# Kernel optimization log

Measured on AMD Instinct MI355X. Metric: run time of the kernel, lower is better.

The kernel has to match this reference:

```python
import jax, jax.numpy as jnp
import numpy as np
from jax import lax

COST_CLASS, COST_BBOX, COST_GIOU = 1.0, 5.0, 2.0


def box_cxcywh_to_xyxy(b):
    cx, cy, w, h = b[..., 0], b[..., 1], b[..., 2], b[..., 3]
    return jnp.stack([cx - 0.5 * w, cy - 0.5 * h, cx + 0.5 * w, cy + 0.5 * h], axis=-1)


def generalized_box_iou(boxes1, boxes2):
    # boxes1: [Q,4] xyxy, boxes2: [T,4] xyxy -> [Q,T]
    area1 = (boxes1[:, 2] - boxes1[:, 0]) * (boxes1[:, 3] - boxes1[:, 1])
    area2 = (boxes2[:, 2] - boxes2[:, 0]) * (boxes2[:, 3] - boxes2[:, 1])
    lt = jnp.maximum(boxes1[:, None, :2], boxes2[None, :, :2])  # [Q,T,2]
    rb = jnp.minimum(boxes1[:, None, 2:], boxes2[None, :, 2:])
    wh = jnp.clip(rb - lt, 0.0)
    inter = wh[..., 0] * wh[..., 1]
    union = area1[:, None] + area2[None, :] - inter
    iou = inter / union
    # smallest enclosing box
    lt_c = jnp.minimum(boxes1[:, None, :2], boxes2[None, :, :2])
    rb_c = jnp.maximum(boxes1[:, None, 2:], boxes2[None, :, 2:])
    wh_c = jnp.clip(rb_c - lt_c, 0.0)
    area_c = wh_c[..., 0] * wh_c[..., 1]
    return iou - (area_c - union) / area_c


def cost_matrix(logits, pboxes, labels, tboxes):
    # logits [Q,C], pboxes [Q,4], labels [T], tboxes [T,4] -> C [Q,T]
    prob = jax.nn.softmax(logits, axis=-1)
    cost_class = -prob[:, labels]                                  # [Q,T]
    cost_bbox = jnp.sum(jnp.abs(pboxes[:, None] - tboxes[None]), axis=-1)  # L1 cdist
    giou = generalized_box_iou(box_cxcywh_to_xyxy(pboxes), box_cxcywh_to_xyxy(tboxes))
    return COST_CLASS * cost_class + COST_BBOX * cost_bbox - COST_GIOU * giou


def greedy_match(C):
    # sequential greedy global-argmin matching, T steps (T <= Q)
    Q, T = C.shape

    def step(Cc, _):
        flat = jnp.argmin(Cc)
        i, j = flat // T, flat % T
        Cc = Cc.at[i, :].set(jnp.inf).at[:, j].set(jnp.inf)
        return Cc, (i.astype(jnp.int32), j.astype(jnp.int32))

    _, (src, tgt) = lax.scan(step, C, None, length=T)
    return src, tgt


def setup_inputs() -> dict:
    key = jax.random.key(0)
    k1, k2, k3, k4 = jax.random.split(key, 4)
    B, Q, C, T = 64, 900, 91, 128
    return {
        "pred_logits": jax.random.normal(k1, (B, Q, C), dtype=jnp.float32),
        "pred_boxes": jax.random.uniform(k2, (B, Q, 4), dtype=jnp.float32),
        "tgt_labels": jax.random.randint(k3, (B, T), 0, C, dtype=jnp.int32),
        "tgt_boxes": jax.random.uniform(k4, (B, T, 4), dtype=jnp.float32),
    }


def reference(pred_logits, pred_boxes, tgt_labels, tgt_boxes):
    C = jax.vmap(cost_matrix)(pred_logits, pred_boxes, tgt_labels, tgt_boxes)  # [B,Q,T]
    src_idx, tgt_idx = jax.vmap(greedy_match)(C)  # [B,T] each
    return src_idx, tgt_idx, C
```

## Files before the change

### kernel.cpp

```cpp
#include <hip/hip_runtime.h>
#include <cstdint>
#include <math.h>

#define NQ 900
#define NT 128
#define NC 91
#define KROWS 15
#define NCH 10

typedef unsigned long long u64;
typedef unsigned int u32;

__device__ __forceinline__ u32 fmono(float f){
  u32 u = __float_as_uint(f);
  return (u & 0x80000000u) ? ~u : (u | 0x80000000u);
}
__device__ __forceinline__ float fmono_inv(u32 m){
  u32 u = (m & 0x80000000u) ? (m & 0x7FFFFFFFu) : ~m;
  return __uint_as_float(u);
}

__device__ __forceinline__ u32 wave_argmin(float lv, u32 lm, float* gout){
  float x = lv;
  #define FSTG(C,RM) { int t_ = __builtin_amdgcn_update_dpp(__float_as_int(x), __float_as_int(x), C, RM, 0xf, false); x = fminf(x, __int_as_float(t_)); }
  FSTG(0x111,0xf) FSTG(0x112,0xf) FSTG(0x114,0xf) FSTG(0x118,0xf)
  FSTG(0x142,0xa) FSTG(0x143,0xc)
  #undef FSTG
  float gv = __int_as_float(__builtin_amdgcn_readlane(__float_as_int(x), 63));
  *gout = gv;
  u64 tie = __ballot(lv == gv);
  if (__popcll(tie) == 1){
    int w = (int)__ffsll((long long)tie) - 1;
    return (u32)__builtin_amdgcn_readlane((int)lm, w);
  }
  u32 m = (lv == gv) ? lm : 0xFFFFFFFFu;
  #define USTG(C,RM) { u32 t_ = (u32)__builtin_amdgcn_update_dpp((int)m, (int)m, C, RM, 0xf, false); m = t_ < m ? t_ : m; }
  USTG(0x111,0xf) USTG(0x112,0xf) USTG(0x114,0xf) USTG(0x118,0xf)
  USTG(0x142,0xa) USTG(0x143,0xc)
  #undef USTG
  return (u32)__builtin_amdgcn_readlane((int)m, 63);
}

__global__ __launch_bounds__(256) void cost_kernel(const float* __restrict__ logits,
                                                   const float* __restrict__ pboxes,
                                                   const int*   __restrict__ labels,
                                                   const float* __restrict__ tboxes,
                                                   float* __restrict__ Cout){
#pragma clang fp contract(off)
  int blk = blockIdx.x, tid = threadIdx.x;
  int idx = blk * 256 + tid;
  int t   = idx & (NT - 1);
  int bq  = idx >> 7;
  int b   = bq / NQ;
  int wid = tid >> 6, lane = tid & 63;

  __shared__ float sm_m[2], sm_s[2];
  if ((wid & 1) == 0){
    int r = blk * 2 + (wid >> 1);
    const float* row = logits + (size_t)r * NC;
    float v0 = (lane      < NC) ? row[lane]      : -INFINITY;
    float v1 = (lane + 64 < NC) ? row[lane + 64] : -INFINITY;
    float m = fmaxf(v0, v1);
    #pragma unroll
    for (int off = 32; off; off >>= 1) m = fmaxf(m, __shfl_xor(m, off));
    float s = ((lane < NC) ? expf(v0 - m) : 0.0f)
            + ((lane + 64 < NC) ? expf(v1 - m) : 0.0f);
    #pragma unroll
    for (int off = 32; off; off >>= 1) s += __shfl_xor(s, off);
    if (lane == 0){ sm_m[wid >> 1] = m; sm_s[wid >> 1] = s; }
  }
  __syncthreads();
  float m = sm_m[tid >> 7], s = sm_s[tid >> 7];

  int   lab = labels[b*NT + t];
  float l   = logits[(size_t)bq*NC + lab];
  float cclass = -(expf(l - m) / s);

  const float* pb = pboxes + (size_t)bq*4;
  const float* tb = tboxes + ((size_t)b*NT + t)*4;
  float pcx = pb[0], pcy = pb[1], pw = pb[2], ph = pb[3];
  float tcx = tb[0], tcy = tb[1], tw = tb[2], th = tb[3];

  float cbbox = ((fabsf(pcx-tcx) + fabsf(pcy-tcy)) + fabsf(pw-tw)) + fabsf(ph-th);

  float px0 = pcx - 0.5f*pw, py0 = pcy - 0.5f*ph;
  float px1 = pcx + 0.5f*pw, py1 = pcy + 0.5f*ph;
  float tx0 = tcx - 0.5f*tw, ty0 = tcy - 0.5f*th;
  float tx1 = tcx + 0.5f*tw, ty1 = tcy + 0.5f*th;

  float area1 = (px1 - px0) * (py1 - py0);
  float area2 = (tx1 - tx0) * (ty1 - ty0);
  float ltx = fmaxf(px0, tx0), lty = fmaxf(py0, ty0);
  float rbx = fminf(px1, tx1), rby = fminf(py1, ty1);
  float wx = fmaxf(rbx - ltx, 0.0f), wy = fmaxf(rby - lty, 0.0f);
  float inter = wx * wy;
  float uni   = (area1 + area2) - inter;
  float iou   = inter / uni;
  float cx0 = fminf(px0, tx0), cy0 = fminf(py0, ty0);
  float cx1 = fmaxf(px1, tx1), cy1 = fmaxf(py1, ty1);
  float cwx = fmaxf(cx1 - cx0, 0.0f), cwy = fmaxf(cy1 - cy0, 0.0f);
  float areac = cwx * cwy;
  float giou  = iou - (areac - uni) / areac;

  float cost = (cclass + 5.0f*cbbox) - 2.0f*giou;
  Cout[idx] = cost;
}

__global__ __launch_bounds__(128) void colmin_kernel(const float* __restrict__ Cmat,
                                                     u64* __restrict__ part){
  int b  = blockIdx.x / NCH;
  int ch = blockIdx.x - b * NCH;
  int t  = threadIdx.x;
  const float* Cb = Cmat + (size_t)b * NQ * NT + t;
  int r0 = ch * (NQ / NCH);
  u64 best = ~0ull;
  #pragma unroll 6
  for (int r = r0; r < r0 + NQ/NCH; ++r){
    float v = Cb[(size_t)r * NT];
    u64 k = ((u64)fmono(v) << 32) | (u32)r;
    best = k < best ? k : best;
  }
  part[((size_t)b * NCH + ch) * NT + t] = best;
}

__global__ __launch_bounds__(64) void greedy_kernel(const float* __restrict__ Cmat,
                                                    const u64* __restrict__ part,
                                                    float* __restrict__ outsrc,
                                                    float* __restrict__ outtgt){
  const int b    = blockIdx.x;
  const int lane = threadIdx.x;
  const float* Cb = Cmat + (size_t)b * NQ * NT;
  const u32 colA = 2*lane, colB = 2*lane + 1;

  u64 kA = ~0ull, kB = ~0ull;
  #pragma unroll
  for (int ch = 0; ch < NCH; ++ch){
    ulonglong2 p = ((const ulonglong2*)(part + ((size_t)b * NCH + ch) * NT))[lane];
    kA = p.x < kA ? p.x : kA;
    kB = p.y < kB ? p.y : kB;
  }
  float vA = fmono_inv((u32)(kA >> 32));
  float vB = fmono_inv((u32)(kB >> 32));
  u32 mA = ((((u32)kA) & 0x3FFu) << 7) | colA;
  u32 mB = ((((u32)kB) & 0x3FFu) << 7) | colB;

  u64 rd[KROWS];
  #pragma unroll
  for (int k = 0; k < KROWS; ++k) rd[k] = 0;

  for (int step = 0; step < NT; ++step){
    u32 gm;
    while (true){
      bool bsel = (vB < vA) || ((vB == vA) && (mB < mA));
      float lv = bsel ? vB : vA;
      u32   lm = bsel ? mB : mA;
      float gv;
      u32 g = wave_argmin(lv, lm, &gv);
      if (!(g >> 24)){ gm = g; break; }

      int jj = (int)(g & 0x7Fu);
      float w1 = INFINITY; u32 s1 = 0;
      #pragma unroll
      for (int k = 0; k < KROWS; ++k){
        int r = lane + 64*k;
        if (r < NQ){
          float v = Cb[(size_t)r * NT + jj];
          bool dead = ((rd[k] >> lane) & 1ull) != 0ull;
          v = dead ? INFINITY : v;
          if (v < w1){ w1 = v; s1 = (u32)r; }
        }
      }
      float rgv;
      u32 rrow = wave_argmin(w1, s1, &rgv);
      if (lane == (jj >> 1)){
        if (jj & 1){ vB = rgv; mB = (rrow << 7) | (u32)jj; }
        else       { vA = rgv; mA = (rrow << 7) | (u32)jj; }
      }
    }

    int i = (int)((gm >> 7) & 0x3FFu);
    int j = (int)(gm & 0x7Fu);
    if (lane == 0){
      outsrc[b*NT + step] = (float)i;
      outtgt[b*NT + step] = (float)j;
    }

    #pragma unroll
    for (int k = 0; k < KROWS; ++k)
      if ((i >> 6) == k) rd[k] |= (1ull << (i & 63));

    if (lane == (j >> 1)){
      if (j & 1){ vB = INFINITY; mB = 0x00FFFFFFu & ~(1u<<24); mB = 0x00FFFFFFu; }
      else      { vA = INFINITY; mA = 0x00FFFFFFu; }
    }
    if (((mA >> 7) & 0x3FFu) == (u32)i) mA |= (1u << 24);
    if (((mB >> 7) & 0x3FFu) == (u32)i) mB |= (1u << 24);
  }
}

extern "C" void kernel_launch(void* const* d_in, const int* in_sizes, int n_in,
                              void* d_out, int out_size, void* d_ws, size_t ws_size,
                              hipStream_t stream){
  const float* logits = (const float*)d_in[0];
  const float* pboxes = (const float*)d_in[1];
  const int*   labels = (const int*)  d_in[2];
  const float* tboxes = (const float*)d_in[3];
  int B = in_sizes[0] / (NQ * NC);

  float* out    = (float*)d_out;
  float* outsrc = out;
  float* outtgt = out + (size_t)B * NT;
  float* Cmat   = out + (size_t)2 * B * NT;

  u64* part = (u64*)d_ws;

  int nblk = (B * NQ) / 2;
  cost_kernel<<<nblk, 256, 0, stream>>>(logits, pboxes, labels, tboxes, Cmat);

  colmin_kernel<<<B * NCH, 128, 0, stream>>>(Cmat, part);

  greedy_kernel<<<B, 64, 0, stream>>>(Cmat, part, outsrc, outtgt);
}
```

Baseline: 246.0 us.

## Fuse cost and column-min kernels, split softmax stats, dual-pop greedy steps

Softmax row statistics move into their own kernel, and the cost computation is fused with the per-chunk column-min reduction, so the cost matrix is no longer re-read by a separate colmin pass. The greedy kernel now tries to commit two matches per iteration when the second argmin cannot conflict with the first. Outputs are buffered in registers and written once at the end. In exchange, the fused kernel launches only B*NCH blocks of 128 threads, far fewer than the old cost kernel, so the GPU may be underfilled. The dual-pop hazard logic also adds correctness risk.

Result: slower. 281.2 us (+14.3%).

```diff
diff --git a/kernel.cpp b/kernel.cpp
--- a/kernel.cpp
+++ b/kernel.cpp
@@ -7,6 +7,7 @@
 #define NC 91
 #define KROWS 15
 #define NCH 10
+#define RPC 90
 
 typedef unsigned long long u64;
 typedef unsigned int u32;
@@ -41,86 +42,75 @@
   return (u32)__builtin_amdgcn_readlane((int)m, 63);
 }
 
-__global__ __launch_bounds__(256) void cost_kernel(const float* __restrict__ logits,
-                                                   const float* __restrict__ pboxes,
-                                                   const int*   __restrict__ labels,
-                                                   const float* __restrict__ tboxes,
-                                                   float* __restrict__ Cout){
+__global__ void softmax_stats_kernel(const float* __restrict__ logits,
+                                     float* __restrict__ stats, int nrows){
+  int gw   = (int)((blockIdx.x * blockDim.x + threadIdx.x) >> 6);
+  int lane = threadIdx.x & 63;
+  if (gw >= nrows) return;
+  const float* row = logits + (size_t)gw * NC;
+  float v0 = (lane      < NC) ? row[lane]      : -INFINITY;
+  float v1 = (lane + 64 < NC) ? row[lane + 64] : -INFINITY;
+  float m = fmaxf(v0, v1);
+  #pragma unroll
+  for (int off = 32; off; off >>= 1) m = fmaxf(m, __shfl_xor(m, off));
+  float s = ((lane < NC) ? expf(v0 - m) : 0.0f)
+          + ((lane + 64 < NC) ? expf(v1 - m) : 0.0f);
+  #pragma unroll
+  for (int off = 32; off; off >>= 1) s += __shfl_xor(s, off);
+  if (lane == 0){ stats[2*gw] = m; stats[2*gw+1] = s; }
+}
+
+__global__ __launch_bounds__(128) void cost_colmin_kernel(
+    const float* __restrict__ logits, const float* __restrict__ pboxes,
+    const int*   __restrict__ labels, const float* __restrict__ tboxes,
+    const float* __restrict__ stats,  float* __restrict__ Cout,
+    u64* __restrict__ part){
 #pragma clang fp contract(off)
-  int blk = blockIdx.x, tid = threadIdx.x;
-  int idx = blk * 256 + tid;
-  int t   = idx & (NT - 1);
-  int bq  = idx >> 7;
-  int b   = bq / NQ;
-  int wid = tid >> 6, lane = tid & 63;
-
-  __shared__ float sm_m[2], sm_s[2];
-  if ((wid & 1) == 0){
-    int r = blk * 2 + (wid >> 1);
-    const float* row = logits + (size_t)r * NC;
-    float v0 = (lane      < NC) ? row[lane]      : -INFINITY;
-    float v1 = (lane + 64 < NC) ? row[lane + 64] : -INFINITY;
-    float m = fmaxf(v0, v1);
-    #pragma unroll
-    for (int off = 32; off; off >>= 1) m = fmaxf(m, __shfl_xor(m, off));
-    float s = ((lane < NC) ? expf(v0 - m) : 0.0f)
-            + ((lane + 64 < NC) ? expf(v1 - m) : 0.0f);
-    #pragma unroll
-    for (int off = 32; off; off >>= 1) s += __shfl_xor(s, off);
-    if (lane == 0){ sm_m[wid >> 1] = m; sm_s[wid >> 1] = s; }
-  }
-  __syncthreads();
-  float m = sm_m[tid >> 7], s = sm_s[tid >> 7];
+  int blk = blockIdx.x;
+  int b = blk / NCH, ch = blk - b * NCH;
+  int t = threadIdx.x;
 
   int   lab = labels[b*NT + t];
-  float l   = logits[(size_t)bq*NC + lab];
-  float cclass = -(expf(l - m) / s);
-
-  const float* pb = pboxes + (size_t)bq*4;
-  const float* tb = tboxes + ((size_t)b*NT + t)*4;
-  float pcx = pb[0], pcy = pb[1], pw = pb[2], ph = pb[3];
-  float tcx = tb[0], tcy = tb[1], tw = tb[2], th = tb[3];
-
-  float cbbox = ((fabsf(pcx-tcx) + fabsf(pcy-tcy)) + fabsf(pw-tw)) + fabsf(ph-th);
-
-  float px0 = pcx - 0.5f*pw, py0 = pcy - 0.5f*ph;
-  float px1 = pcx + 0.5f*pw, py1 = pcy + 0.5f*ph;
+  float4 tb4 = ((const float4*)tboxes)[b*NT + t];
+  float tcx = tb4.x, tcy = tb4.y, tw = tb4.z, th = tb4.w;
   float tx0 = tcx - 0.5f*tw, ty0 = tcy - 0.5f*th;
   float tx1 = tcx + 0.5f*tw, ty1 = tcy + 0.5f*th;
-
-  float area1 = (px1 - px0) * (py1 - py0);
   float area2 = (tx1 - tx0) * (ty1 - ty0);
-  float ltx = fmaxf(px0, tx0), lty = fmaxf(py0, ty0);
-  float rbx = fminf(px1, tx1), rby = fminf(py1, ty1);
-  float wx = fmaxf(rbx - ltx, 0.0f), wy = fmaxf(rby - lty, 0.0f);
-  float inter = wx * wy;
-  float uni   = (area1 + area2) - inter;
-  float iou   = inter / uni;
-  float cx0 = fminf(px0, tx0), cy0 = fminf(py0, ty0);
-  float cx1 = fmaxf(px1, tx1), cy1 = fmaxf(py1, ty1);
-  float cwx = fmaxf(cx1 - cx0, 0.0f), cwy = fmaxf(cy1 - cy0, 0.0f);
-  float areac = cwx * cwy;
-  float giou  = iou - (areac - uni) / areac;
-
-  float cost = (cclass + 5.0f*cbbox) - 2.0f*giou;
-  Cout[idx] = cost;
-}
-
-__global__ __launch_bounds__(128) void colmin_kernel(const float* __restrict__ Cmat,
-                                                     u64* __restrict__ part){
-  int b  = blockIdx.x / NCH;
-  int ch = blockIdx.x - b * NCH;
-  int t  = threadIdx.x;
-  const float* Cb = Cmat + (size_t)b * NQ * NT + t;
-  int r0 = ch * (NQ / NCH);
+
+  int r0 = ch * RPC;
   u64 best = ~0ull;
-  #pragma unroll 6
-  for (int r = r0; r < r0 + NQ/NCH; ++r){
-    float v = Cb[(size_t)r * NT];
-    u64 k = ((u64)fmono(v) << 32) | (u32)r;
+  for (int rr = 0; rr < RPC; ++rr){
+    int q = r0 + rr;
+    size_t bq = (size_t)b*NQ + q;
+    float m = stats[2*bq], s = stats[2*bq+1];
+    float4 pb4 = ((const float4*)pboxes)[bq];
+    float pcx = pb4.x, pcy = pb4.y, pw = pb4.z, ph = pb4.w;
+    float l = logits[bq*NC + lab];
+    float cclass = -(expf(l - m) / s);
+
+    float cbbox = ((fabsf(pcx-tcx) + fabsf(pcy-tcy)) + fabsf(pw-tw)) + fabsf(ph-th);
+
+    float px0 = pcx - 0.5f*pw, py0 = pcy - 0.5f*ph;
+    float px1 = pcx + 0.5f*pw, py1 = pcy + 0.5f*ph;
+    float area1 = (px1 - px0) * (py1 - py0);
+    float ltx = fmaxf(px0, tx0), lty = fmaxf(py0, ty0);
+    float rbx = fminf(px1, tx1), rby = fminf(py1, ty1);
+    float wx = fmaxf(rbx - ltx, 0.0f), wy = fmaxf(rby - lty, 0.0f);
+    float inter = wx * wy;
+    float uni   = (area1 + area2) - inter;
+    float iou   = inter / uni;
+    float cx0 = fminf(px0, tx0), cy0 = fminf(py0, ty0);
+    float cx1 = fmaxf(px1, tx1), cy1 = fmaxf(py1, ty1);
+    float cwx = fmaxf(cx1 - cx0, 0.0f), cwy = fmaxf(cy1 - cy0, 0.0f);
+    float areac = cwx * cwy;
+    float giou  = iou - (areac - uni) / areac;
+
+    float cost = (cclass + 5.0f*cbbox) - 2.0f*giou;
+    Cout[bq*NT + t] = cost;
+    u64 k = ((u64)fmono(cost) << 32) | (u32)q;
     best = k < best ? k : best;
   }
-  part[((size_t)b * NCH + ch) * NT + t] = best;
+  part[((size_t)b*NCH + ch)*NT + t] = best;
 }
 
 __global__ __launch_bounds__(64) void greedy_kernel(const float* __restrict__ Cmat,
@@ -148,17 +138,18 @@
   #pragma unroll
   for (int k = 0; k < KROWS; ++k) rd[k] = 0;
 
-  for (int step = 0; step < NT; ++step){
-    u32 gm;
+  int so0 = 0, so1 = 0, to0 = 0, to1 = 0;
+
+  int step = 0;
+  while (step < NT){
+    u32 g1; float gv1;
     while (true){
       bool bsel = (vB < vA) || ((vB == vA) && (mB < mA));
       float lv = bsel ? vB : vA;
       u32   lm = bsel ? mB : mA;
-      float gv;
-      u32 g = wave_argmin(lv, lm, &gv);
-      if (!(g >> 24)){ gm = g; break; }
-
-      int jj = (int)(g & 0x7Fu);
+      g1 = wave_argmin(lv, lm, &gv1);
+      if (!(g1 >> 24)) break;
+      int jj = (int)(g1 & 0x7Fu);
       float w1 = INFINITY; u32 s1 = 0;
       #pragma unroll
       for (int k = 0; k < KROWS; ++k){
@@ -170,32 +161,71 @@
           if (v < w1){ w1 = v; s1 = (u32)r; }
         }
       }
-      float rgv;
-      u32 rrow = wave_argmin(w1, s1, &rgv);
+      float rgv; u32 rrow = wave_argmin(w1, s1, &rgv);
       if (lane == (jj >> 1)){
         if (jj & 1){ vB = rgv; mB = (rrow << 7) | (u32)jj; }
         else       { vA = rgv; mA = (rrow << 7) | (u32)jj; }
       }
     }
-
-    int i = (int)((gm >> 7) & 0x3FFu);
-    int j = (int)(gm & 0x7Fu);
-    if (lane == 0){
-      outsrc[b*NT + step] = (float)i;
-      outtgt[b*NT + step] = (float)j;
+    int i1 = (int)((g1 >> 7) & 0x3FFu);
+    int j1 = (int)(g1 & 0x7Fu);
+    if (step < 64){ if (lane == step)      { so0 = i1; to0 = j1; } }
+    else          { if (lane == step - 64) { so1 = i1; to1 = j1; } }
+
+    int npop = 1, i2 = 0, j2 = 0;
+    if (step + 1 < NT){
+      float lv2; u32 lm2;
+      if (lane == (j1 >> 1)){
+        if (j1 & 1){ lv2 = vA; lm2 = mA; } else { lv2 = vB; lm2 = mB; }
+      } else {
+        bool bs2 = (vB < vA) || ((vB == vA) && (mB < mA));
+        lv2 = bs2 ? vB : vA;
+        lm2 = bs2 ? mB : mA;
+      }
+      float gv2; u32 g2 = wave_argmin(lv2, lm2, &gv2);
+      int r2 = (int)((g2 >> 7) & 0x3FFu);
+      bool hzA = (vA == gv2) && (((mA >> 7) & 0x3FFu) == (u32)i1) && (colA != (u32)j1);
+      bool hzB = (vB == gv2) && (((mB >> 7) & 0x3FFu) == (u32)i1) && (colB != (u32)j1);
+      bool anyhz = __ballot(hzA || hzB) != 0ull;
+      if (!(g2 >> 24) && r2 != i1 && !anyhz){
+        i2 = r2; j2 = (int)(g2 & 0x7Fu);
+        int s2 = step + 1;
+        if (s2 < 64){ if (lane == s2)      { so0 = i2; to0 = j2; } }
+        else        { if (lane == s2 - 64) { so1 = i2; to1 = j2; } }
+        npop = 2;
+      }
     }
 
     #pragma unroll
     for (int k = 0; k < KROWS; ++k)
-      if ((i >> 6) == k) rd[k] |= (1ull << (i & 63));
-
-    if (lane == (j >> 1)){
-      if (j & 1){ vB = INFINITY; mB = 0x00FFFFFFu & ~(1u<<24); mB = 0x00FFFFFFu; }
-      else      { vA = INFINITY; mA = 0x00FFFFFFu; }
-    }
-    if (((mA >> 7) & 0x3FFu) == (u32)i) mA |= (1u << 24);
-    if (((mB >> 7) & 0x3FFu) == (u32)i) mB |= (1u << 24);
-  }
+      if ((i1 >> 6) == k) rd[k] |= (1ull << (i1 & 63));
+    if (lane == (j1 >> 1)){
+      if (j1 & 1){ vB = INFINITY; mB = 0x00FFFFFFu; }
+      else       { vA = INFINITY; mA = 0x00FFFFFFu; }
+    }
+    if (((mA >> 7) & 0x3FFu) == (u32)i1) mA |= (1u << 24);
+    if (((mB >> 7) & 0x3FFu) == (u32)i1) mB |= (1u << 24);
+
+    if (npop == 2){
+      #pragma unroll
+      for (int k = 0; k < KROWS; ++k)
+        if ((i2 >> 6) == k) rd[k] |= (1ull << (i2 & 63));
+      if (lane == (j2 >> 1)){
+        if (j2 & 1){ vB = INFINITY; mB = 0x00FFFFFFu; }
+        else       { vA = INFINITY; mA = 0x00FFFFFFu; }
+      }
+      if (((mA >> 7) & 0x3FFu) == (u32)i2) mA |= (1u << 24);
+      if (((mB >> 7) & 0x3FFu) == (u32)i2) mB |= (1u << 24);
+    }
+    step += npop;
+  }
+
+  float* os = outsrc + b*NT;
+  float* ot = outtgt + b*NT;
+  os[lane]      = (float)so0;
+  os[64 + lane] = (float)so1;
+  ot[lane]      = (float)to0;
+  ot[64 + lane] = (float)to1;
 }
 
 extern "C" void kernel_launch(void* const* d_in, const int* in_sizes, int n_in,
@@ -212,12 +242,15 @@
   float* outtgt = out + (size_t)B * NT;
   float* Cmat   = out + (size_t)2 * B * NT;
 
-  u64* part = (u64*)d_ws;
-
-  int nblk = (B * NQ) / 2;
-  cost_kernel<<<nblk, 256, 0, stream>>>(logits, pboxes, labels, tboxes, Cmat);
-
-  colmin_kernel<<<B * NCH, 128, 0, stream>>>(Cmat, part);
+  u64*   part  = (u64*)d_ws;
+  float* stats = (float*)((char*)d_ws + (size_t)B * NCH * NT * sizeof(u64));
+
+  int nrows = B * NQ;
+  int blocks0 = (nrows + 3) / 4;
+  softmax_stats_kernel<<<blocks0, 256, 0, stream>>>(logits, stats, nrows);
+
+  cost_colmin_kernel<<<B * NCH, 128, 0, stream>>>(logits, pboxes, labels,
+                                                  tboxes, stats, Cmat, part);
 
   greedy_kernel<<<B, 64, 0, stream>>>(Cmat, part, outsrc, outtgt);
 }
```
